# Performance work log

Measured on AMD Instinct MI355X. Metric: run time of the kernel, lower is better.

## Reference

```python
import jax, jax.numpy as jnp
import numpy as np

T, H = 1024, 2048          # tokens, hidden_size
E, K = 8, 4                # num_experts, top_k
I_E = 1408                 # moe_intermediate_size
I_S = 5632                 # shared_expert_intermediate_size


def setup_inputs() -> dict:
    key = jax.random.key(0)
    ks = jax.random.split(key, 7)
    s = 0.02
    return {
        "hidden_states": jax.random.normal(ks[0], (T, H), dtype=jnp.float32),
        "w_gate": jax.random.normal(ks[1], (H, E), dtype=jnp.float32) * s,
        "w_shared_gate": jax.random.normal(ks[2], (H, 1), dtype=jnp.float32) * s,
        "w_shared_gu": jax.random.normal(ks[3], (H, 2 * I_S), dtype=jnp.float32) * s,
        "w_shared_down": jax.random.normal(ks[4], (I_S, H), dtype=jnp.float32) * s,
        "w_exp_gu": jax.random.normal(ks[5], (E, H, 2 * I_E), dtype=jnp.float32) * s,
        "w_exp_down": jax.random.normal(ks[6], (E, I_E, H), dtype=jnp.float32) * s,
    }


def _silu_and_mul(gu):
    g, u = jnp.split(gu, 2, axis=-1)
    return jax.nn.silu(g) * u


def reference(hidden_states, w_gate, w_shared_gate, w_shared_gu, w_shared_down,
              w_exp_gu, w_exp_down):
    x = hidden_states  # [T, H]

    # ---- router: softmax -> top_k (norm_topk_prob=False, no renormalize) ----
    router_logits = x @ w_gate                       # [T, E]
    probs = jax.nn.softmax(router_logits, axis=-1)
    topw, topi = jax.lax.top_k(probs, K)             # [T, K] each
    # per-token combine weights over experts: [T, E]
    comb = jnp.sum(jax.nn.one_hot(topi, E, dtype=probs.dtype) * topw[..., None], axis=1)

    # ---- fused experts (dense-per-expert reference for grouped GEMM) ----
    gu = jnp.einsum('th,ehf->etf', x, w_exp_gu)      # [E, T, 2*I_E]
    act = _silu_and_mul(gu)                          # [E, T, I_E]
    out_e = jnp.einsum('etf,efh->eth', act, w_exp_down)  # [E, T, H]
    fused_out = jnp.einsum('eth,te->th', out_e, comb)    # [T, H]

    # ---- shared expert with sigmoid gate ----
    s_act = _silu_and_mul(x @ w_shared_gu)           # [T, I_S]
    shared_out = s_act @ w_shared_down               # [T, H]
    shared_out = jax.nn.sigmoid(x @ w_shared_gate) * shared_out

    return shared_out + fused_out
```

## Files before the change

kernel.cpp:

```cpp
#include <hip/hip_runtime.h>
#include <hip/hip_bf16.h>
#include <stdint.h>

#define T_TOK 1024
#define H_DIM 2048
#define NEXP 8
#define IED 1408
#define ISD 5632

typedef __attribute__((ext_vector_type(8))) short s16x8;
typedef __attribute__((ext_vector_type(8))) unsigned short u16x8;
typedef __attribute__((ext_vector_type(4))) float f32x4;

#define SWZ(r) (((r) ^ ((r) >> 2)) & 3)

__device__ __forceinline__ unsigned short f2bf(float f) {
  union { float f; unsigned u; } v; v.f = f;
  unsigned r = v.u + 0x7FFFu + ((v.u >> 16) & 1u);
  return (unsigned short)(r >> 16);
}

__device__ __forceinline__ void gload16(const void* g, void* l) {
  __builtin_amdgcn_global_load_lds(
      (const __attribute__((address_space(1))) unsigned int*)g,
      (__attribute__((address_space(3))) unsigned int*)l, 16, 0, 0);
}

extern "C" __global__ void __launch_bounds__(256) k_router(
    const float* __restrict__ x, const float* __restrict__ wg,
    const float* __restrict__ wsg, unsigned short* __restrict__ xb,
    int* __restrict__ counts, int* __restrict__ tlist,
    float* __restrict__ wlist, float* __restrict__ gate_sig) {
  const int tid = threadIdx.x;
  const int bb = blockIdx.x;
#pragma unroll
  for (int it = 0; it < 8; it++) {
    int i = bb * 8192 + it * 1024 + tid * 4;
    float4 v = *(const float4*)(x + i);
    ushort4 o;
    o.x = f2bf(v.x); o.y = f2bf(v.y); o.z = f2bf(v.z); o.w = f2bf(v.w);
    *(ushort4*)(xb + i) = o;
  }
  const int lane = tid & 63;
  const int t = bb * 4 + (tid >> 6);
  const float* xr = x + (size_t)t * H_DIM;
  float acc[8];
#pragma unroll
  for (int e = 0; e < 8; e++) acc[e] = 0.f;
  float sg = 0.f;
  for (int h = lane; h < H_DIM; h += 64) {
    float xv = xr[h];
    float4 w0 = *(const float4*)(wg + h * 8);
    float4 w1 = *(const float4*)(wg + h * 8 + 4);
    acc[0] += xv * w0.x; acc[1] += xv * w0.y; acc[2] += xv * w0.z; acc[3] += xv * w0.w;
    acc[4] += xv * w1.x; acc[5] += xv * w1.y; acc[6] += xv * w1.z; acc[7] += xv * w1.w;
    sg += xv * wsg[h];
  }
#pragma unroll
  for (int d = 32; d >= 1; d >>= 1) {
#pragma unroll
    for (int e = 0; e < 8; e++) acc[e] += __shfl_xor(acc[e], d, 64);
    sg += __shfl_xor(sg, d, 64);
  }
  if (lane == 0) {
    float m = acc[0];
#pragma unroll
    for (int e = 1; e < 8; e++) m = fmaxf(m, acc[e]);
    float p[8], s = 0.f;
#pragma unroll
    for (int e = 0; e < 8; e++) { p[e] = __expf(acc[e] - m); s += p[e]; }
    float inv = 1.f / s;
    bool used[8];
#pragma unroll
    for (int e = 0; e < 8; e++) used[e] = false;
    for (int j = 0; j < 4; j++) {
      int be = 0; float bv = -1e30f;
#pragma unroll
      for (int e = 0; e < 8; e++)
        if (!used[e] && acc[e] > bv) { bv = acc[e]; be = e; }
      used[be] = true;
      int slot = atomicAdd(counts + be, 1);
      tlist[be * T_TOK + slot] = t;
      wlist[be * T_TOK + slot] = p[be] * inv;
    }
    gate_sig[t] = 1.f / (1.f + __expf(-sg));
  }
}

#define ISSUE_A(kk, OFFS)                                                 \
  do {                                                                    \
    _Pragma("unroll") for (int q = 0; q < 2; q++)                         \
        gload16(asrc[q] + (kk), adst[q] + (OFFS));                        \
    __builtin_amdgcn_sched_barrier(0);                                    \
  } while (0)

#define ISSUE_B(kk)                                                       \
  do {                                                                    \
    _Pragma("unroll") for (int i = 0; i < 8; i++)                         \
        RB[i] = *(const float2*)(Bh + (size_t)((kk) + bks + i) * (size_t)ldb + bn); \
  } while (0)

#define CVTB(OFFS)                                                        \
  do {                                                                    \
    _Pragma("unroll") for (int jj = 0; jj < 2; jj++) {                    \
      u16x8 pk;                                                           \
      _Pragma("unroll") for (int i = 0; i < 8; i++)                       \
          pk[i] = f2bf(jj ? RB[i].y : RB[i].x);                           \
      *(u16x8*)(bwr[jj] + (OFFS)) = pk;                                   \
    }                                                                     \
  } while (0)

#define COMPUTE(OFFS)                                                     \
  do {                                                                    \
    const unsigned short* ab = a_lds + (OFFS);                            \
    const unsigned short* bb2 = b_lds + (OFFS);                           \
    __builtin_amdgcn_s_setprio(1);                                        \
    {                                                                     \
      const int kc = lane >> 4;                                           \
      s16x8 afr[4];                                                       \
      _Pragma("unroll") for (int m = 0; m < 4; m++) {                     \
        int r = wm * 64 + m * 16 + (lane & 15);                           \
        afr[m] = *(const s16x8*)&ab[r * 32 + ((kc ^ SWZ(r)) * 8)];        \
      }                                                                   \
      _Pragma("unroll") for (int nf = 0; nf < 4; nf++) {                  \
        int rb_;                                                          \
        if constexpr (DOWN) rb_ = wn * 64 + nf * 16;                      \
        else rb_ = wn * 32 + (nf & 1) * 16 + (nf >> 1) * 64;              \
        rb_ += (lane & 15);                                               \
        s16x8 bfr = *(const s16x8*)&bb2[rb_ * 32 + ((kc ^ SWZ(rb_)) * 8)]; \
        _Pragma("unroll") for (int m = 0; m < 4; m++)                     \
            acc[m][nf] = __builtin_amdgcn_mfma_f32_16x16x32_bf16(         \
                afr[m], bfr, acc[m][nf], 0, 0, 0);                        \
      }                                                                   \
    }                                                                     \
    __builtin_amdgcn_s_setprio(0);                                        \
  } while (0)

template <int DOWN>
__global__ void __launch_bounds__(256, 4) k_mm(
    const unsigned short* __restrict__ A_sh, const unsigned short* __restrict__ A_ex,
    const float* __restrict__ B_sh, const float* __restrict__ B_ex,
    unsigned short* __restrict__ act_sh, unsigned short* __restrict__ act_ex,
    float* __restrict__ out,
    const int* __restrict__ counts, const int* __restrict__ tlist,
    const float* __restrict__ wlist, const float* __restrict__ gate_sig) {
  const int tid = threadIdx.x;
  const int lane = tid & 63;
  const int wid = tid >> 6;
  const int wm = wid >> 1, wn = wid & 1;

  constexpr int SHBLK = DOWN ? 512 : 704;
  const int b0 = blockIdx.x;
  const bool ex = b0 >= SHBLK;
  const int b = ex ? b0 - SHBLK : b0;
  const int xcd = b & 7;
  const int j = b >> 3;
  const int mtile = j & 7;
  int e = 0, ntile = 0, z = 0;
  if constexpr (!DOWN) {
    if (!ex) ntile = xcd * 11 + (j >> 3);
    else { int p = xcd * 22 + (j >> 3); e = p & 7; ntile = p >> 3; }
  } else {
    if (!ex) { int p = xcd * 8 + (j >> 3); ntile = p >> 2; z = p & 3; }
    else { int p = xcd * 16 + (j >> 3); e = p & 7; ntile = p >> 3; }
  }

  int lda, ldb, IK = 0, kbeg = 0, count = T_TOK;
  const unsigned short* A;
  const float* B0; const float* B1;
  const int* tlA = nullptr;
  const int* tlO = nullptr;
  const float* wl = nullptr;
  unsigned short* actout = nullptr;

  if constexpr (!DOWN) {
    lda = H_DIM;
    if (!ex) {
      ldb = 2 * ISD; IK = ISD; A = A_sh; actout = act_sh;
      B0 = B_sh + ntile * 64; B1 = B_sh + ISD + ntile * 64;
    } else {
      count = counts[e];
      if (mtile * 128 >= count) return;
      ldb = 2 * IED; IK = IED; A = A_sh;
      const float* Bw = B_ex + (size_t)e * H_DIM * (2 * IED);
      B0 = Bw + ntile * 64; B1 = Bw + IED + ntile * 64;
      tlA = tlist + e * T_TOK; wl = wlist + e * T_TOK;
      actout = act_ex + (size_t)e * T_TOK * IED;
    }
  } else {
    ldb = H_DIM;
    if (!ex) {
      lda = ISD; kbeg = z * 1408; A = A_sh;
      B0 = B_sh + ntile * 128; B1 = B0 + 64;
    } else {
      count = counts[e];
      if (mtile * 128 >= count) return;
      lda = IED; A = A_ex + (size_t)e * T_TOK * IED;
      B0 = B_ex + (size_t)e * IED * H_DIM + ntile * 128; B1 = B0 + 64;
      tlO = tlist + e * T_TOK;
    }
  }
  const int nt = DOWN ? 44 : 64;

  __shared__ unsigned short a_lds[2 * 4096];
  __shared__ unsigned short b_lds[2 * 4096];

  const unsigned short* asrc[2];
  unsigned short* adst[2];
#pragma unroll
  for (int q = 0; q < 2; q++) {
    int row = wid * 32 + q * 16 + (lane >> 2);
    int rowg = mtile * 128 + row;
    int arow = rowg;
    if (tlA) arow = tlA[rowg];
    asrc[q] = A + (size_t)arow * lda + (((lane & 3) ^ SWZ(row)) * 8);
    adst[q] = &a_lds[(wid * 32 + q * 16) * 32];
  }

  const int half = tid >> 7;
  const int bn = (tid & 31) * 2;
  const int kg = (tid >> 5) & 3;
  const int bks = kg * 8;
  const float* Bh = half ? B1 : B0;
  unsigned short* bwr[2];
#pragma unroll
  for (int jj = 0; jj < 2; jj++) {
    int r = half * 64 + bn + jj;
    bwr[jj] = &b_lds[r * 32 + ((kg ^ SWZ(r)) * 8)];
  }

  const f32x4 fzero = {0.f, 0.f, 0.f, 0.f};
  f32x4 acc[4][4];
#pragma unroll
  for (int m = 0; m < 4; m++)
#pragma unroll
    for (int n = 0; n < 4; n++) acc[m][n] = fzero;

  float2 RB[8];

  ISSUE_B(kbeg);
  ISSUE_A(kbeg, 0);
  CVTB(0);
  ISSUE_B(kbeg + 32);
  __builtin_amdgcn_sched_barrier(0);
  asm volatile("s_waitcnt vmcnt(8)" ::: "memory");
  asm volatile("s_waitcnt lgkmcnt(0)" ::: "memory");
  __builtin_amdgcn_s_barrier();
  __builtin_amdgcn_sched_barrier(0);

  for (int u = 0; u < nt; ++u) {
    const int cur = (u & 1) * 4096;
    const int nxt = cur ^ 4096;
    const int k0 = kbeg + u * 32;
    const bool haveN1 = (u + 1 < nt);
    const bool haveN2 = (u + 2 < nt);
    if (haveN1) {
      ISSUE_A(k0 + 32, nxt);
      CVTB(nxt);
      if (haveN2) ISSUE_B(k0 + 64);
    }
    COMPUTE(cur);
    if (haveN1) {
      __builtin_amdgcn_sched_barrier(0);
      if (haveN2)
        asm volatile("s_waitcnt vmcnt(8)" ::: "memory");
      else
        asm volatile("s_waitcnt vmcnt(0)" ::: "memory");
      asm volatile("s_waitcnt lgkmcnt(0)" ::: "memory");
      __builtin_amdgcn_s_barrier();
      __builtin_amdgcn_sched_barrier(0);
    }
  }

  if constexpr (!DOWN) {
#pragma unroll
    for (int m = 0; m < 4; m++) {
#pragma unroll
      for (int i = 0; i < 4; i++) {
        int rowslot = mtile * 128 + wm * 64 + m * 16 + (lane >> 4) * 4 + i;
        float rsc = 1.f;
        if (wl) rsc = wl[rowslot];
#pragma unroll
        for (int p = 0; p < 2; p++) {
          float g = acc[m][p][i];
          float u2 = acc[m][p + 2][i];
          float sv = g / (1.f + __expf(-g)) * u2 * rsc;
          int col = ntile * 64 + wn * 32 + p * 16 + (lane & 15);
          actout[(size_t)rowslot * IK + col] = f2bf(sv);
        }
      }
    }
  } else {
#pragma unroll
    for (int m = 0; m < 4; m++) {
#pragma unroll
      for (int i = 0; i < 4; i++) {
        int rowslot = mtile * 128 + wm * 64 + m * 16 + (lane >> 4) * 4 + i;
        int token = rowslot;
        if (tlO) token = tlO[rowslot];
        float sc = ex ? 1.f : gate_sig[token];
        float* orow = out + (size_t)token * H_DIM + ntile * 128 + wn * 64 + (lane & 15);
#pragma unroll
        for (int nf = 0; nf < 4; nf++)
          atomicAdd(orow + nf * 16, acc[m][nf][i] * sc);
      }
    }
  }
}

extern "C" void kernel_launch(void* const* d_in, const int* in_sizes, int n_in,
                              void* d_out, int out_size, void* d_ws, size_t ws_size,
                              hipStream_t stream) {
  (void)in_sizes; (void)n_in; (void)out_size; (void)ws_size;
  const float* x    = (const float*)d_in[0];
  const float* wg   = (const float*)d_in[1];
  const float* wsg  = (const float*)d_in[2];
  const float* wsgu = (const float*)d_in[3];
  const float* wsd  = (const float*)d_in[4];
  const float* wegu = (const float*)d_in[5];
  const float* wed  = (const float*)d_in[6];
  float* out = (float*)d_out;

  char* ws = (char*)d_ws;
  unsigned short* xb   = (unsigned short*)ws;
  unsigned short* acts = (unsigned short*)(ws + (4u << 20));
  unsigned short* acte = (unsigned short*)(ws + (4u << 20) + 11534336u);
  char* ctrl = ws + (4u << 20) + 11534336u + 23068672u;
  int* counts    = (int*)ctrl;
  int* tlist     = (int*)(ctrl + 256);
  float* wlist   = (float*)(ctrl + 256 + 32768);
  float* gate_sig = (float*)(ctrl + 256 + 65536);

  hipMemsetAsync(d_out, 0, (size_t)T_TOK * H_DIM * 4, stream);
  hipMemsetAsync(ctrl, 0, 256 + 65536, stream);

  k_router<<<dim3(256), dim3(256), 0, stream>>>(x, wg, wsg, xb, counts, tlist, wlist, gate_sig);
  k_mm<0><<<dim3(2112), dim3(256), 0, stream>>>(xb, xb, wsgu, wegu, acts, acte, nullptr,
                                                counts, tlist, wlist, gate_sig);
  k_mm<1><<<dim3(1536), dim3(256), 0, stream>>>(acts, acte, wsd, wed, nullptr, nullptr, out,
                                                counts, tlist, wlist, gate_sig);
}
```

Before: 467.8 us.

## Deepen GEMM pipeline to triple-buffered LDS with padded B stride

Replaces the two-stage double-buffered K loop with a three-stage pipeline. A tiles are prefetched two steps ahead and B register sets three steps ahead, rotating through three LDS buffers and three register sets, with adjusted vmcnt thresholds. The B tile in LDS switches from an XOR swizzle to a padded row stride of 36. The bf16 conversion now uses the HIP intrinsic. Launch bounds drop from 4 to 3 blocks per CU to fit the larger LDS and register footprint. This trades occupancy and registers for hiding more global-load latency.

```diff
diff --git a/kernel.cpp b/kernel.cpp
--- a/kernel.cpp
+++ b/kernel.cpp
@@ -13,11 +13,14 @@
 typedef __attribute__((ext_vector_type(4))) float f32x4;
 
 #define SWZ(r) (((r) ^ ((r) >> 2)) & 3)
+#define BSTR 36
+#define A_OFF(i) ((i) * 4096)
+#define B_OFF(i) ((i) * 4608)
 
 __device__ __forceinline__ unsigned short f2bf(float f) {
-  union { float f; unsigned u; } v; v.f = f;
-  unsigned r = v.u + 0x7FFFu + ((v.u >> 16) & 1u);
-  return (unsigned short)(r >> 16);
+  union { __hip_bfloat16 b; unsigned short u; } v;
+  v.b = __float2bfloat16(f);
+  return v.u;
 }
 
 __device__ __forceinline__ void gload16(const void* g, void* l) {
@@ -87,33 +90,34 @@
   }
 }
 
-#define ISSUE_A(kk, OFFS)                                                 \
+#define ISSUE_A(kk, AOFF)                                                 \
   do {                                                                    \
     _Pragma("unroll") for (int q = 0; q < 2; q++)                         \
-        gload16(asrc[q] + (kk), adst[q] + (OFFS));                        \
+        gload16(asrc[q] + (kk), adst[q] + (AOFF));                        \
     __builtin_amdgcn_sched_barrier(0);                                    \
   } while (0)
 
-#define ISSUE_B(kk)                                                       \
+#define ISSUE_B(SET, kk)                                                  \
   do {                                                                    \
     _Pragma("unroll") for (int i = 0; i < 8; i++)                         \
-        RB[i] = *(const float2*)(Bh + (size_t)((kk) + bks + i) * (size_t)ldb + bn); \
-  } while (0)
-
-#define CVTB(OFFS)                                                        \
+        SET[i] = *(const float2*)(Bh + (size_t)((kk) + bks + i) * (size_t)ldb + bn); \
+    __builtin_amdgcn_sched_barrier(0);                                    \
+  } while (0)
+
+#define CVTB(SET, BOFF)                                                   \
   do {                                                                    \
     _Pragma("unroll") for (int jj = 0; jj < 2; jj++) {                    \
       u16x8 pk;                                                           \
       _Pragma("unroll") for (int i = 0; i < 8; i++)                       \
-          pk[i] = f2bf(jj ? RB[i].y : RB[i].x);                           \
-      *(u16x8*)(bwr[jj] + (OFFS)) = pk;                                   \
+          pk[i] = f2bf(jj ? SET[i].y : SET[i].x);                         \
+      *(u16x8*)(bwr[jj] + (BOFF)) = pk;                                   \
     }                                                                     \
   } while (0)
 
-#define COMPUTE(OFFS)                                                     \
-  do {                                                                    \
-    const unsigned short* ab = a_lds + (OFFS);                            \
-    const unsigned short* bb2 = b_lds + (OFFS);                           \
+#define COMPUTE(AOFF, BOFF)                                               \
+  do {                                                                    \
+    const unsigned short* ab = a_lds + (AOFF);                            \
+    const unsigned short* bb2 = b_lds + (BOFF);                           \
     __builtin_amdgcn_s_setprio(1);                                        \
     {                                                                     \
       const int kc = lane >> 4;                                           \
@@ -127,7 +131,7 @@
         if constexpr (DOWN) rb_ = wn * 64 + nf * 16;                      \
         else rb_ = wn * 32 + (nf & 1) * 16 + (nf >> 1) * 64;              \
         rb_ += (lane & 15);                                               \
-        s16x8 bfr = *(const s16x8*)&bb2[rb_ * 32 + ((kc ^ SWZ(rb_)) * 8)]; \
+        s16x8 bfr = *(const s16x8*)&bb2[rb_ * BSTR + kc * 8];             \
         _Pragma("unroll") for (int m = 0; m < 4; m++)                     \
             acc[m][nf] = __builtin_amdgcn_mfma_f32_16x16x32_bf16(         \
                 afr[m], bfr, acc[m][nf], 0, 0, 0);                        \
@@ -136,8 +140,29 @@
     __builtin_amdgcn_s_setprio(0);                                        \
   } while (0)
 
+#define STEP(UU, S0, S1, S2, I0, I1, I2)                                  \
+  do {                                                                    \
+    const int u_ = (UU);                                                  \
+    if (u_ + 2 < nt) ISSUE_A(kbeg + (u_ + 2) * 32, A_OFF(I2));            \
+    if (u_ + 3 < nt) ISSUE_B(S0, kbeg + (u_ + 3) * 32);                   \
+    if (u_ + 1 < nt) CVTB(S1, B_OFF(I1));                                 \
+    COMPUTE(A_OFF(I0), B_OFF(I0));                                        \
+    if (u_ + 1 < nt) {                                                    \
+      __builtin_amdgcn_sched_barrier(0);                                  \
+      if (u_ + 3 < nt)                                                    \
+        asm volatile("s_waitcnt vmcnt(18)" ::: "memory");                 \
+      else if (u_ + 2 < nt)                                               \
+        asm volatile("s_waitcnt vmcnt(10)" ::: "memory");                 \
+      else                                                                \
+        asm volatile("s_waitcnt vmcnt(0)" ::: "memory");                  \
+      asm volatile("s_waitcnt lgkmcnt(0)" ::: "memory");                  \
+      __builtin_amdgcn_s_barrier();                                       \
+      __builtin_amdgcn_sched_barrier(0);                                  \
+    }                                                                     \
+  } while (0)
+
 template <int DOWN>
-__global__ void __launch_bounds__(256, 4) k_mm(
+__global__ void __launch_bounds__(256, 3) k_mm(
     const unsigned short* __restrict__ A_sh, const unsigned short* __restrict__ A_ex,
     const float* __restrict__ B_sh, const float* __restrict__ B_ex,
     unsigned short* __restrict__ act_sh, unsigned short* __restrict__ act_ex,
@@ -202,8 +227,8 @@
   }
   const int nt = DOWN ? 44 : 64;
 
-  __shared__ unsigned short a_lds[2 * 4096];
-  __shared__ unsigned short b_lds[2 * 4096];
+  __shared__ unsigned short a_lds[3 * 4096];
+  __shared__ unsigned short b_lds[3 * 4608];
 
   const unsigned short* asrc[2];
   unsigned short* adst[2];
@@ -226,7 +251,7 @@
 #pragma unroll
   for (int jj = 0; jj < 2; jj++) {
     int r = half * 64 + bn + jj;
-    bwr[jj] = &b_lds[r * 32 + ((kg ^ SWZ(r)) * 8)];
+    bwr[jj] = &b_lds[r * BSTR + kg * 8];
   }
 
   const f32x4 fzero = {0.f, 0.f, 0.f, 0.f};
@@ -236,40 +261,23 @@
 #pragma unroll
     for (int n = 0; n < 4; n++) acc[m][n] = fzero;
 
-  float2 RB[8];
-
-  ISSUE_B(kbeg);
-  ISSUE_A(kbeg, 0);
-  CVTB(0);
-  ISSUE_B(kbeg + 32);
+  float2 RB0[8], RB1[8], RB2[8];
+
+  ISSUE_A(kbeg, A_OFF(0));
+  ISSUE_B(RB0, kbeg);
+  ISSUE_A(kbeg + 32, A_OFF(1));
+  ISSUE_B(RB1, kbeg + 32);
+  CVTB(RB0, B_OFF(0));
+  ISSUE_B(RB2, kbeg + 64);
   __builtin_amdgcn_sched_barrier(0);
-  asm volatile("s_waitcnt vmcnt(8)" ::: "memory");
   asm volatile("s_waitcnt lgkmcnt(0)" ::: "memory");
   __builtin_amdgcn_s_barrier();
   __builtin_amdgcn_sched_barrier(0);
 
-  for (int u = 0; u < nt; ++u) {
-    const int cur = (u & 1) * 4096;
-    const int nxt = cur ^ 4096;
-    const int k0 = kbeg + u * 32;
-    const bool haveN1 = (u + 1 < nt);
-    const bool haveN2 = (u + 2 < nt);
-    if (haveN1) {
-      ISSUE_A(k0 + 32, nxt);
-      CVTB(nxt);
-      if (haveN2) ISSUE_B(k0 + 64);
-    }
-    COMPUTE(cur);
-    if (haveN1) {
-      __builtin_amdgcn_sched_barrier(0);
-      if (haveN2)
-        asm volatile("s_waitcnt vmcnt(8)" ::: "memory");
-      else
-        asm volatile("s_waitcnt vmcnt(0)" ::: "memory");
-      asm volatile("s_waitcnt lgkmcnt(0)" ::: "memory");
-      __builtin_amdgcn_s_barrier();
-      __builtin_amdgcn_sched_barrier(0);
-    }
+  for (int u = 0; u < nt; u += 3) {
+    STEP(u,     RB0, RB1, RB2, 0, 1, 2);
+    if (u + 1 < nt) STEP(u + 1, RB1, RB2, RB0, 1, 2, 0);
+    if (u + 2 < nt) STEP(u + 2, RB2, RB0, RB1, 2, 0, 1);
   }
 
   if constexpr (!DOWN) {
```

Measured after the change: 1.084 ms. 132% more time.

## Double GEMM block to 512 threads with 2x4 wave layout and per-thread B loads

Applied to the files above, without the earlier changes.

The GEMM kernels now launch 512 threads per block, arranged as 2x4 waves, so each wave owns a 64x32 output slice with half the accumulators. A and B staging is redistributed so each thread issues one global-to-LDS A load and eight scalar fp32 B loads per k-step, replacing the float2 loads. The manual bf16 rounding is swapped for the HIP intrinsic, and the launch_bounds occupancy hint is removed. The aim is more waves in flight to hide latency, but each wave gets less MFMA work per LDS fragment read, and the narrower B loads may lower memory efficiency.

```diff
diff --git a/kernel.cpp b/kernel.cpp
--- a/kernel.cpp
+++ b/kernel.cpp
@@ -15,9 +15,9 @@
 #define SWZ(r) (((r) ^ ((r) >> 2)) & 3)
 
 __device__ __forceinline__ unsigned short f2bf(float f) {
-  union { float f; unsigned u; } v; v.f = f;
-  unsigned r = v.u + 0x7FFFu + ((v.u >> 16) & 1u);
-  return (unsigned short)(r >> 16);
+  union { __hip_bfloat16 b; unsigned short u; } v;
+  v.b = __float2bfloat16(f);
+  return v.u;
 }
 
 __device__ __forceinline__ void gload16(const void* g, void* l) {
@@ -87,33 +87,30 @@
   }
 }
 
-#define ISSUE_A(kk, OFFS)                                                 \
+#define ISSUE_A(kk, AOFF)                                                 \
   do {                                                                    \
-    _Pragma("unroll") for (int q = 0; q < 2; q++)                         \
-        gload16(asrc[q] + (kk), adst[q] + (OFFS));                        \
+    gload16(asrc + (kk), adst + (AOFF));                                  \
     __builtin_amdgcn_sched_barrier(0);                                    \
   } while (0)
 
 #define ISSUE_B(kk)                                                       \
   do {                                                                    \
-    _Pragma("unroll") for (int i = 0; i < 8; i++)                         \
-        RB[i] = *(const float2*)(Bh + (size_t)((kk) + bks + i) * (size_t)ldb + bn); \
+    _Pragma("unroll") for (int j = 0; j < 8; j++)                         \
+        RB[j] = Bh[(size_t)((kk) + bc * 8 + j) * (size_t)ldb];            \
+    __builtin_amdgcn_sched_barrier(0);                                    \
   } while (0)
 
-#define CVTB(OFFS)                                                        \
+#define CVTB(BOFF)                                                        \
   do {                                                                    \
-    _Pragma("unroll") for (int jj = 0; jj < 2; jj++) {                    \
-      u16x8 pk;                                                           \
-      _Pragma("unroll") for (int i = 0; i < 8; i++)                       \
-          pk[i] = f2bf(jj ? RB[i].y : RB[i].x);                           \
-      *(u16x8*)(bwr[jj] + (OFFS)) = pk;                                   \
-    }                                                                     \
+    u16x8 pk;                                                             \
+    _Pragma("unroll") for (int j = 0; j < 8; j++) pk[j] = f2bf(RB[j]);    \
+    *(u16x8*)(bwr + (BOFF)) = pk;                                         \
   } while (0)
 
-#define COMPUTE(OFFS)                                                     \
+#define COMPUTE(AOFF, BOFF)                                               \
   do {                                                                    \
-    const unsigned short* ab = a_lds + (OFFS);                            \
-    const unsigned short* bb2 = b_lds + (OFFS);                           \
+    const unsigned short* ab = a_lds + (AOFF);                            \
+    const unsigned short* bb2 = b_lds + (BOFF);                           \
     __builtin_amdgcn_s_setprio(1);                                        \
     {                                                                     \
       const int kc = lane >> 4;                                           \
@@ -122,11 +119,8 @@
         int r = wm * 64 + m * 16 + (lane & 15);                           \
         afr[m] = *(const s16x8*)&ab[r * 32 + ((kc ^ SWZ(r)) * 8)];        \
       }                                                                   \
-      _Pragma("unroll") for (int nf = 0; nf < 4; nf++) {                  \
-        int rb_;                                                          \
-        if constexpr (DOWN) rb_ = wn * 64 + nf * 16;                      \
-        else rb_ = wn * 32 + (nf & 1) * 16 + (nf >> 1) * 64;              \
-        rb_ += (lane & 15);                                               \
+      _Pragma("unroll") for (int nf = 0; nf < 2; nf++) {                  \
+        int rb_ = wn * 16 + nf * 64 + (lane & 15);                        \
         s16x8 bfr = *(const s16x8*)&bb2[rb_ * 32 + ((kc ^ SWZ(rb_)) * 8)]; \
         _Pragma("unroll") for (int m = 0; m < 4; m++)                     \
             acc[m][nf] = __builtin_amdgcn_mfma_f32_16x16x32_bf16(         \
@@ -137,7 +131,7 @@
   } while (0)
 
 template <int DOWN>
-__global__ void __launch_bounds__(256, 4) k_mm(
+__global__ void k_mm(
     const unsigned short* __restrict__ A_sh, const unsigned short* __restrict__ A_ex,
     const float* __restrict__ B_sh, const float* __restrict__ B_ex,
     unsigned short* __restrict__ act_sh, unsigned short* __restrict__ act_ex,
@@ -147,7 +141,7 @@
   const int tid = threadIdx.x;
   const int lane = tid & 63;
   const int wid = tid >> 6;
-  const int wm = wid >> 1, wn = wid & 1;
+  const int wm = wid >> 2, wn = wid & 3;
 
   constexpr int SHBLK = DOWN ? 512 : 704;
   const int b0 = blockIdx.x;
@@ -165,78 +159,71 @@
     else { int p = xcd * 16 + (j >> 3); e = p & 7; ntile = p >> 3; }
   }
 
-  int lda, ldb, IK = 0, kbeg = 0, count = T_TOK;
+  int lda, ldb, IK = 0, kbeg = 0, count = T_TOK, nt;
   const unsigned short* A;
-  const float* B0; const float* B1;
+  const float* Bb0; const float* Bb1;
   const int* tlA = nullptr;
   const int* tlO = nullptr;
   const float* wl = nullptr;
   unsigned short* actout = nullptr;
 
   if constexpr (!DOWN) {
-    lda = H_DIM;
+    lda = H_DIM; nt = 64;
     if (!ex) {
       ldb = 2 * ISD; IK = ISD; A = A_sh; actout = act_sh;
-      B0 = B_sh + ntile * 64; B1 = B_sh + ISD + ntile * 64;
+      Bb0 = B_sh + ntile * 64; Bb1 = B_sh + ISD + ntile * 64;
     } else {
       count = counts[e];
       if (mtile * 128 >= count) return;
       ldb = 2 * IED; IK = IED; A = A_sh;
       const float* Bw = B_ex + (size_t)e * H_DIM * (2 * IED);
-      B0 = Bw + ntile * 64; B1 = Bw + IED + ntile * 64;
+      Bb0 = Bw + ntile * 64; Bb1 = Bw + IED + ntile * 64;
       tlA = tlist + e * T_TOK; wl = wlist + e * T_TOK;
       actout = act_ex + (size_t)e * T_TOK * IED;
     }
   } else {
-    ldb = H_DIM;
+    ldb = H_DIM; nt = 44;
     if (!ex) {
       lda = ISD; kbeg = z * 1408; A = A_sh;
-      B0 = B_sh + ntile * 128; B1 = B0 + 64;
+      Bb0 = B_sh + ntile * 128; Bb1 = Bb0;
     } else {
       count = counts[e];
       if (mtile * 128 >= count) return;
       lda = IED; A = A_ex + (size_t)e * T_TOK * IED;
-      B0 = B_ex + (size_t)e * IED * H_DIM + ntile * 128; B1 = B0 + 64;
+      Bb0 = B_ex + (size_t)e * IED * H_DIM + ntile * 128; Bb1 = Bb0;
       tlO = tlist + e * T_TOK;
     }
   }
-  const int nt = DOWN ? 44 : 64;
 
   __shared__ unsigned short a_lds[2 * 4096];
   __shared__ unsigned short b_lds[2 * 4096];
 
-  const unsigned short* asrc[2];
-  unsigned short* adst[2];
-#pragma unroll
-  for (int q = 0; q < 2; q++) {
-    int row = wid * 32 + q * 16 + (lane >> 2);
+  const unsigned short* asrc;
+  unsigned short* adst;
+  {
+    int row = tid >> 2;
     int rowg = mtile * 128 + row;
     int arow = rowg;
     if (tlA) arow = tlA[rowg];
-    asrc[q] = A + (size_t)arow * lda + (((lane & 3) ^ SWZ(row)) * 8);
-    adst[q] = &a_lds[(wid * 32 + q * 16) * 32];
-  }
-
-  const int half = tid >> 7;
-  const int bn = (tid & 31) * 2;
-  const int kg = (tid >> 5) & 3;
-  const int bks = kg * 8;
-  const float* Bh = half ? B1 : B0;
-  unsigned short* bwr[2];
-#pragma unroll
-  for (int jj = 0; jj < 2; jj++) {
-    int r = half * 64 + bn + jj;
-    bwr[jj] = &b_lds[r * 32 + ((kg ^ SWZ(r)) * 8)];
-  }
+    asrc = A + (size_t)arow * lda + (((tid & 3) ^ SWZ(row)) * 8);
+    adst = &a_lds[(tid >> 6) * 512];
+  }
+
+  const int bnn = tid & 127;
+  const int bc = tid >> 7;
+  const float* Bh;
+  if constexpr (!DOWN) Bh = (bnn < 64) ? (Bb0 + bnn) : (Bb1 + (bnn - 64));
+  else Bh = Bb0 + bnn;
+  unsigned short* bwr = &b_lds[bnn * 32 + ((bc ^ SWZ(bnn)) * 8)];
 
   const f32x4 fzero = {0.f, 0.f, 0.f, 0.f};
-  f32x4 acc[4][4];
+  f32x4 acc[4][2];
 #pragma unroll
   for (int m = 0; m < 4; m++)
 #pragma unroll
-    for (int n = 0; n < 4; n++) acc[m][n] = fzero;
-
-  float2 RB[8];
+    for (int n = 0; n < 2; n++) acc[m][n] = fzero;
+
+  float RB[8];
 
   ISSUE_B(kbeg);
   ISSUE_A(kbeg, 0);
@@ -259,7 +246,7 @@
       CVTB(nxt);
       if (haveN2) ISSUE_B(k0 + 64);
     }
-    COMPUTE(cur);
+    COMPUTE(cur, cur);
     if (haveN1) {
       __builtin_amdgcn_sched_barrier(0);
       if (haveN2)
@@ -280,14 +267,11 @@
         int rowslot = mtile * 128 + wm * 64 + m * 16 + (lane >> 4) * 4 + i;
         float rsc = 1.f;
         if (wl) rsc = wl[rowslot];
-#pragma unroll
-        for (int p = 0; p < 2; p++) {
-          float g = acc[m][p][i];
-          float u2 = acc[m][p + 2][i];
-          float sv = g / (1.f + __expf(-g)) * u2 * rsc;
-          int col = ntile * 64 + wn * 32 + p * 16 + (lane & 15);
-          actout[(size_t)rowslot * IK + col] = f2bf(sv);
-        }
+        float g = acc[m][0][i];
+        float u2 = acc[m][1][i];
+        float sv = g / (1.f + __expf(-g)) * u2 * rsc;
+        int col = ntile * 64 + wn * 16 + (lane & 15);
+        actout[(size_t)rowslot * IK + col] = f2bf(sv);
       }
     }
   } else {
@@ -299,10 +283,10 @@
         int token = rowslot;
         if (tlO) token = tlO[rowslot];
         float sc = ex ? 1.f : gate_sig[token];
-        float* orow = out + (size_t)token * H_DIM + ntile * 128 + wn * 64 + (lane & 15);
-#pragma unroll
-        for (int nf = 0; nf < 4; nf++)
-          atomicAdd(orow + nf * 16, acc[m][nf][i] * sc);
+        float* orow = out + (size_t)token * H_DIM + ntile * 128 + wn * 16 + (lane & 15);
+#pragma unroll
+        for (int nf = 0; nf < 2; nf++)
+          atomicAdd(orow + nf * 64, acc[m][nf][i] * sc);
       }
     }
   }
@@ -335,8 +319,8 @@
   hipMemsetAsync(ctrl, 0, 256 + 65536, stream);
 
   k_router<<<dim3(256), dim3(256), 0, stream>>>(x, wg, wsg, xb, counts, tlist, wlist, gate_sig);
-  k_mm<0><<<dim3(2112), dim3(256), 0, stream>>>(xb, xb, wsgu, wegu, acts, acte, nullptr,
+  k_mm<0><<<dim3(2112), dim3(512), 0, stream>>>(xb, xb, wsgu, wegu, acts, acte, nullptr,
                                                 counts, tlist, wlist, gate_sig);
-  k_mm<1><<<dim3(1536), dim3(256), 0, stream>>>(acts, acte, wsd, wed, nullptr, nullptr, out,
+  k_mm<1><<<dim3(1536), dim3(512), 0, stream>>>(acts, acte, wsd, wed, nullptr, nullptr, out,
                                                 counts, tlist, wlist, gate_sig);
 }
```

After: 472.0 us. No clear change (+0.9%).
